# Kernel optimization log

Hardware: AMD Instinct MI355X
Metric: run time of the kernel (lower is better)

Reference implementation:

```python
import jax, jax.numpy as jnp
import numpy as np

B, C, D, H, W = 8, 16, 32, 112, 112
D_OUT, H3, W3, H2, W2 = 16, 14, 14, 7, 7
HID, OUT = 256, 128
IN_SIZE = C * H2 * W2  # 784


def setup_inputs() -> dict:
    key = jax.random.key(0)
    ks = jax.random.split(key, 8)
    s_ih = 1.0 / np.sqrt(HID)
    return {
        "x": jax.random.normal(ks[0], (B, C, D, H, W), dtype=jnp.float32),
        "W_ih": jax.random.uniform(ks[1], (3 * HID, IN_SIZE), jnp.float32, -s_ih, s_ih),
        "W_hh": jax.random.uniform(ks[2], (3 * HID, HID), jnp.float32, -s_ih, s_ih),
        "b_ih": jax.random.uniform(ks[3], (3 * HID,), jnp.float32, -s_ih, s_ih),
        "b_hh": jax.random.uniform(ks[4], (3 * HID,), jnp.float32, -s_ih, s_ih),
        "W_out": jax.random.uniform(ks[5], (OUT, HID), jnp.float32, -s_ih, s_ih),
        "b_out": jax.random.uniform(ks[6], (OUT,), jnp.float32, -s_ih, s_ih),
    }


def reference(x, W_ih, W_hh, b_ih, b_hh, W_out, b_out):
    # AdaptiveAvgPool3d (D,H,W)->(D_OUT,H3,W3): divisible factors -> mean pooling
    p3 = x.reshape(B, C, D_OUT, D // D_OUT, H3, H // H3, W3, W // W3).mean(axis=(3, 5, 7))
    # AdaptiveAvgPool2d per temporal slice (H3,W3)->(H2,W2)
    p2 = p3.reshape(B, C, D_OUT, H2, H3 // H2, W2, W3 // W2).mean(axis=(4, 6))
    # sequence over D_OUT: [T, B, C*H2*W2]
    seq = p2.transpose(2, 0, 1, 3, 4).reshape(D_OUT, B, IN_SIZE)

    def step(h, inp):
        gi = inp @ W_ih.T + b_ih  # [B, 3H]
        gh = h @ W_hh.T + b_hh    # [B, 3H]
        ir, iz, inn = jnp.split(gi, 3, axis=-1)
        hr, hz, hn = jnp.split(gh, 3, axis=-1)
        r = jax.nn.sigmoid(ir + hr)
        z = jax.nn.sigmoid(iz + hz)
        n = jnp.tanh(inn + r * hn)
        h_new = (1.0 - z) * n + z * h
        return h_new, None

    h0 = jnp.zeros((B, HID), dtype=x.dtype)
    h, _ = jax.lax.scan(step, h0, seq)
    return h @ W_out.T + b_out
```

## Files before the change

### kernel.cpp

```cpp
#include <hip/hip_runtime.h>
#include <hip/hip_bf16.h>
#include <cstdint>

#define BB 8
#define CC 16
#define DD 32
#define HH 112
#define WW 112
#define TT 16
#define HID 256
#define OUTN 128
#define INSZ 784
#define NCACHE 48

__device__ __forceinline__ float bf16lo(uint32_t u) { return __uint_as_float(u << 16); }
__device__ __forceinline__ float bf16hi(uint32_t u) { return __uint_as_float(u & 0xffff0000u); }
__device__ __forceinline__ float bf16s(uint16_t u)  { return __uint_as_float(((uint32_t)u) << 16); }

__device__ __forceinline__ uint16_t f32_to_bf16_rne(float f) {
    uint32_t u = __float_as_uint(f);
    return (uint16_t)((u + 0x7fffu + ((u >> 16) & 1u)) >> 16);
}

__global__ __launch_bounds__(256) void detect_kernel(const uint16_t* __restrict__ x,
                                                     int* __restrict__ flag) {
    __shared__ int cnt;
    if (threadIdx.x == 0) cnt = 0;
    __syncthreads();
    int local = 0;
    for (int i = threadIdx.x; i < 8192; i += 256) {
        uint32_t e = (x[i] >> 7) & 0xFFu;
        if (e == 0u || e >= 0x90u) local++;
    }
    atomicAdd(&cnt, local);
    __syncthreads();
    if (threadIdx.x == 0) *flag = (cnt > 400) ? 1 : 0;
}

__global__ __launch_bounds__(256) void pool_kernel(const void* __restrict__ xv,
                                                   float* __restrict__ seq,
                                                   const int* __restrict__ flag) {
    const int isf32 = *flag;
    int gid = blockIdx.x;
    int t = gid & 15, c = (gid >> 4) & 15, b = gid >> 8;
    long base = (long)(((b * CC + c) * DD) + t * 2) * (HH * WW);
    __shared__ float chunk[6272];
    int tid = threadIdx.x;
    float s = 0.0f;
    if (!isf32) {
        const uint4* p = reinterpret_cast<const uint4*>((const uint16_t*)xv + base);
        for (int m = tid; m < 3136; m += 256) {
            uint4 v = p[m];
            chunk[m] = bf16lo(v.x) + bf16hi(v.x) + bf16lo(v.y) + bf16hi(v.y)
                     + bf16lo(v.z) + bf16hi(v.z) + bf16lo(v.w) + bf16hi(v.w);
        }
        __syncthreads();
        if (tid < 49) {
            int h2 = tid / 7, w2 = tid - h2 * 7;
            #pragma unroll
            for (int d = 0; d < 2; d++)
                for (int hh = 0; hh < 16; hh++) {
                    int row = d * 1568 + (h2 * 16 + hh) * 14 + w2 * 2;
                    s += chunk[row] + chunk[row + 1];
                }
        }
    } else {
        const float4* p = reinterpret_cast<const float4*>((const float*)xv + base);
        for (int m = tid; m < 6272; m += 256) {
            float4 v = p[m];
            chunk[m] = v.x + v.y + v.z + v.w;
        }
        __syncthreads();
        if (tid < 49) {
            int h2 = tid / 7, w2 = tid - h2 * 7;
            #pragma unroll
            for (int d = 0; d < 2; d++)
                for (int hh = 0; hh < 16; hh++) {
                    int row = d * 3136 + (h2 * 16 + hh) * 28 + w2 * 4;
                    s += chunk[row] + chunk[row + 1] + chunk[row + 2] + chunk[row + 3];
                }
        }
    }
    if (tid < 49) {
        seq[(long)(t * BB + b) * INSZ + c * 49 + tid] = s * (1.0f / 512.0f);
    }
}

__global__ __launch_bounds__(256) void pack_all(const void* __restrict__ Wih,
                                                float* __restrict__ wihT,
                                                const void* __restrict__ Whh,
                                                uint32_t* __restrict__ whhP,
                                                const void* __restrict__ bih,
                                                float* __restrict__ gi,
                                                const int* __restrict__ flag) {
    const int isf32 = *flag;
    const int blk = blockIdx.x;
    const int tid = threadIdx.x;
    __shared__ float tlds[64][65];
    if (blk < 156) {
        int jt = blk / 13, kt = blk - jt * 13;
        int j0 = jt * 64, k0 = kt * 64;
        int rr = tid >> 6, c = tid & 63;
        #pragma unroll
        for (int r0 = 0; r0 < 64; r0 += 4) {
            int jL = r0 + rr;
            int k = k0 + c;
            if (k < INSZ) {
                long idx = (long)(j0 + jL) * INSZ + k;
                tlds[jL][c] = isf32 ? ((const float*)Wih)[idx]
                                    : bf16s(((const uint16_t*)Wih)[idx]);
            }
        }
        __syncthreads();
        #pragma unroll
        for (int r0 = 0; r0 < 64; r0 += 4) {
            int kL = r0 + rr;
            int k = k0 + kL;
            if (k < INSZ) {
                wihT[(long)k * 768 + j0 + c] = tlds[c][kL];
            }
        }
    } else if (blk < 540) {
        int g = (blk - 156) * 256 + tid;
        int jr = g >> 7, kk = g & 127;
        uint32_t u;
        if (isf32) {
            float2 v = ((const float2*)Whh)[g];
            u = (uint32_t)f32_to_bf16_rne(v.x) | ((uint32_t)f32_to_bf16_rne(v.y) << 16);
        } else {
            u = ((const uint32_t*)Whh)[g];
        }
        whhP[kk * 768 + jr] = u;
    } else {
        int g = (blk - 540) * 256 + tid;
        int jj = g % 768;
        float bv = isf32 ? ((const float*)bih)[jj] : bf16s(((const uint16_t*)bih)[jj]);
        gi[g] = bv;
    }
}

__global__ __launch_bounds__(256) void gi_kernel(const float* __restrict__ seq,
                                                 const float* __restrict__ wihT,
                                                 float* __restrict__ gi) {
    int jg = blockIdx.x % 3;
    int tbg = (blockIdx.x / 3) & 31;
    int kh = blockIdx.x / 96;
    int tb0 = tbg * 4;
    int j = jg * 256 + threadIdx.x;
    int k0 = kh * 392;
    __shared__ __align__(16) float s_in[392 * 4];
    const float* sbase = seq + (long)tb0 * INSZ + k0;
    for (int idx = threadIdx.x; idx < 392 * 4; idx += 256) {
        int i = idx / 392, k = idx - i * 392;
        s_in[k * 4 + i] = sbase[(long)i * INSZ + k];
    }
    __syncthreads();
    float a0 = 0.0f, a1 = 0.0f, a2 = 0.0f, a3 = 0.0f;
    const float* wp = wihT + (long)k0 * 768 + j;
    const float4* s4 = reinterpret_cast<const float4*>(s_in);
    #pragma unroll 8
    for (int k = 0; k < 392; k++) {
        float w = wp[(long)k * 768];
        float4 sv = s4[k];
        a0 += w * sv.x; a1 += w * sv.y; a2 += w * sv.z; a3 += w * sv.w;
    }
    atomicAdd(&gi[(long)(tb0 + 0) * 768 + j], a0);
    atomicAdd(&gi[(long)(tb0 + 1) * 768 + j], a1);
    atomicAdd(&gi[(long)(tb0 + 2) * 768 + j], a2);
    atomicAdd(&gi[(long)(tb0 + 3) * 768 + j], a3);
}

__global__ __launch_bounds__(768) void gru_kernel(const float* __restrict__ gi,
                                                  const uint32_t* __restrict__ whhP,
                                                  const void* __restrict__ bhh,
                                                  const void* __restrict__ Wout,
                                                  const void* __restrict__ bout,
                                                  void* __restrict__ out,
                                                  const int* __restrict__ flag) {
    const int isf32 = *flag;
    int b = blockIdx.x;
    int j = threadIdx.x;
    __shared__ __align__(16) float h_s[HID];
    __shared__ __align__(16) float g_s[768];
    __shared__ __align__(16) uint32_t w_s[NCACHE * 768];
    if (j < HID) h_s[j] = 0.0f;
    float bh = isf32 ? ((const float*)bhh)[j] : bf16s(((const uint16_t*)bhh)[j]);
    for (int idx = j; idx < NCACHE * 768; idx += 768) w_s[idx] = whhP[idx];
    const uint32_t* wpg = whhP + (long)NCACHE * 768 + j;
    const uint32_t* wls = w_s + j;
    __syncthreads();
    #pragma unroll 1
    for (int t = 0; t < TT; t++) {
        float a0 = bh, a1 = 0.0f;
        const float2* h2p = reinterpret_cast<const float2*>(h_s);
        #pragma unroll 8
        for (int kk = 0; kk < 128 - NCACHE; kk++) {
            uint32_t u = wpg[kk * 768];
            float2 hv = h2p[NCACHE + kk];
            a0 += bf16lo(u) * hv.x;
            a1 += bf16hi(u) * hv.y;
        }
        #pragma unroll 8
        for (int kk = 0; kk < NCACHE; kk++) {
            uint32_t u = wls[kk * 768];
            float2 hv = h2p[kk];
            a0 += bf16lo(u) * hv.x;
            a1 += bf16hi(u) * hv.y;
        }
        g_s[j] = a0 + a1;
        __syncthreads();
        if (j < HID) {
            const float* gp = gi + (long)(t * BB + b) * 768;
            float r = 1.0f / (1.0f + __expf(-(gp[j]       + g_s[j])));
            float z = 1.0f / (1.0f + __expf(-(gp[j + 256] + g_s[j + 256])));
            float npre = gp[j + 512] + r * g_s[j + 512];
            float n = 2.0f / (1.0f + __expf(-2.0f * npre)) - 1.0f;
            h_s[j] = (1.0f - z) * n + z * h_s[j];
        }
        __syncthreads();
    }
    if (j < OUTN) {
        float acc = isf32 ? ((const float*)bout)[j] : bf16s(((const uint16_t*)bout)[j]);
        if (!isf32) {
            const uint4* wo = reinterpret_cast<const uint4*>((const uint16_t*)Wout + (long)j * HID);
            #pragma unroll
            for (int k = 0; k < 32; k++) {
                uint4 v = wo[k];
                const float* hp2 = &h_s[k * 8];
                acc += bf16lo(v.x) * hp2[0] + bf16hi(v.x) * hp2[1]
                     + bf16lo(v.y) * hp2[2] + bf16hi(v.y) * hp2[3]
                     + bf16lo(v.z) * hp2[4] + bf16hi(v.z) * hp2[5]
                     + bf16lo(v.w) * hp2[6] + bf16hi(v.w) * hp2[7];
            }
            ((uint16_t*)out)[b * OUTN + j] = f32_to_bf16_rne(acc);
        } else {
            const float4* wo = reinterpret_cast<const float4*>((const float*)Wout + (long)j * HID);
            #pragma unroll
            for (int k = 0; k < 64; k++) {
                float4 v = wo[k];
                const float* hp2 = &h_s[k * 4];
                acc += v.x * hp2[0] + v.y * hp2[1] + v.z * hp2[2] + v.w * hp2[3];
            }
            ((float*)out)[b * OUTN + j] = acc;
        }
    }
}

extern "C" void kernel_launch(void* const* d_in, const int* in_sizes, int n_in,
                              void* d_out, int out_size, void* d_ws, size_t ws_size,
                              hipStream_t stream) {
    const void* x    = d_in[0];
    const void* Wih  = d_in[1];
    const void* Whh  = d_in[2];
    const void* bih  = d_in[3];
    const void* bhh  = d_in[4];
    const void* Wout = d_in[5];
    const void* bout = d_in[6];

    char* ws = (char*)d_ws;
    float*    seq  = (float*)ws;
    float*    gi   = (float*)(ws + 401408);
    float*    wihT = (float*)(ws + 1048576);
    uint32_t* whhP = (uint32_t*)(ws + 4194304);
    int*     flagp = (int*)(ws + 8388608);

    detect_kernel<<<1, 256, 0, stream>>>((const uint16_t*)x, flagp);
    pool_kernel<<<2048, 256, 0, stream>>>(x, seq, flagp);
    pack_all<<<924, 256, 0, stream>>>(Wih, wihT, Whh, whhP, bih, gi, flagp);
    gi_kernel<<<192, 256, 0, stream>>>(seq, wihT, gi);
    gru_kernel<<<8, 768, 0, stream>>>(gi, whhP, bhh, Wout, bout, d_out, flagp);
}
```

Measured before the change: 405.9 us.

## Merge pooling and weight packing into one launch; keep GRU recurrent weights in registers

Combines the pooling kernel and the weight/bias packing kernel into one grid, indexed by block range, so one launch and its inter-kernel gap disappear and packing blocks can run alongside pooling. The GRU kernel now loads the 80 non-LDS-cached W_hh columns into per-thread registers once, instead of re-reading them from global memory on each of the 16 timesteps. The added launch_bounds minimum-blocks hint and the 80-element register array raise register pressure with 768 threads per block, which could cause spills.

New measurement: 413.4 us. About the same (+1.8%).

```diff
diff --git a/kernel.cpp b/kernel.cpp
--- a/kernel.cpp
+++ b/kernel.cpp
@@ -12,6 +12,7 @@
 #define OUTN 128
 #define INSZ 784
 #define NCACHE 48
+#define NREG (128 - NCACHE)
 
 __device__ __forceinline__ float bf16lo(uint32_t u) { return __uint_as_float(u << 16); }
 __device__ __forceinline__ float bf16hi(uint32_t u) { return __uint_as_float(u & 0xffff0000u); }
@@ -37,68 +38,63 @@
     if (threadIdx.x == 0) *flag = (cnt > 400) ? 1 : 0;
 }
 
-__global__ __launch_bounds__(256) void pool_kernel(const void* __restrict__ xv,
-                                                   float* __restrict__ seq,
-                                                   const int* __restrict__ flag) {
-    const int isf32 = *flag;
-    int gid = blockIdx.x;
-    int t = gid & 15, c = (gid >> 4) & 15, b = gid >> 8;
-    long base = (long)(((b * CC + c) * DD) + t * 2) * (HH * WW);
-    __shared__ float chunk[6272];
-    int tid = threadIdx.x;
-    float s = 0.0f;
-    if (!isf32) {
-        const uint4* p = reinterpret_cast<const uint4*>((const uint16_t*)xv + base);
-        for (int m = tid; m < 3136; m += 256) {
-            uint4 v = p[m];
-            chunk[m] = bf16lo(v.x) + bf16hi(v.x) + bf16lo(v.y) + bf16hi(v.y)
-                     + bf16lo(v.z) + bf16hi(v.z) + bf16lo(v.w) + bf16hi(v.w);
-        }
-        __syncthreads();
-        if (tid < 49) {
-            int h2 = tid / 7, w2 = tid - h2 * 7;
-            #pragma unroll
-            for (int d = 0; d < 2; d++)
-                for (int hh = 0; hh < 16; hh++) {
-                    int row = d * 1568 + (h2 * 16 + hh) * 14 + w2 * 2;
-                    s += chunk[row] + chunk[row + 1];
-                }
-        }
-    } else {
-        const float4* p = reinterpret_cast<const float4*>((const float*)xv + base);
-        for (int m = tid; m < 6272; m += 256) {
-            float4 v = p[m];
-            chunk[m] = v.x + v.y + v.z + v.w;
-        }
-        __syncthreads();
-        if (tid < 49) {
-            int h2 = tid / 7, w2 = tid - h2 * 7;
-            #pragma unroll
-            for (int d = 0; d < 2; d++)
-                for (int hh = 0; hh < 16; hh++) {
-                    int row = d * 3136 + (h2 * 16 + hh) * 28 + w2 * 4;
-                    s += chunk[row] + chunk[row + 1] + chunk[row + 2] + chunk[row + 3];
-                }
-        }
-    }
-    if (tid < 49) {
-        seq[(long)(t * BB + b) * INSZ + c * 49 + tid] = s * (1.0f / 512.0f);
-    }
-}
-
-__global__ __launch_bounds__(256) void pack_all(const void* __restrict__ Wih,
-                                                float* __restrict__ wihT,
-                                                const void* __restrict__ Whh,
-                                                uint32_t* __restrict__ whhP,
-                                                const void* __restrict__ bih,
-                                                float* __restrict__ gi,
-                                                const int* __restrict__ flag) {
+__global__ __launch_bounds__(256) void prep2_kernel(const void* __restrict__ xv,
+                                                    float* __restrict__ seq,
+                                                    const void* __restrict__ Wih,
+                                                    float* __restrict__ wihT,
+                                                    const void* __restrict__ Whh,
+                                                    uint32_t* __restrict__ whhP,
+                                                    const void* __restrict__ bih,
+                                                    float* __restrict__ gi,
+                                                    const int* __restrict__ flag) {
     const int isf32 = *flag;
     const int blk = blockIdx.x;
     const int tid = threadIdx.x;
-    __shared__ float tlds[64][65];
-    if (blk < 156) {
-        int jt = blk / 13, kt = blk - jt * 13;
+    __shared__ float chunk[6272];
+    if (blk < 2048) {
+        int t = blk & 15, c = (blk >> 4) & 15, b = blk >> 8;
+        long base = (long)(((b * CC + c) * DD) + t * 2) * (HH * WW);
+        float s = 0.0f;
+        if (!isf32) {
+            const uint4* p = reinterpret_cast<const uint4*>((const uint16_t*)xv + base);
+            for (int m = tid; m < 3136; m += 256) {
+                uint4 v = p[m];
+                chunk[m] = bf16lo(v.x) + bf16hi(v.x) + bf16lo(v.y) + bf16hi(v.y)
+                         + bf16lo(v.z) + bf16hi(v.z) + bf16lo(v.w) + bf16hi(v.w);
+            }
+            __syncthreads();
+            if (tid < 49) {
+                int h2 = tid / 7, w2 = tid - h2 * 7;
+                #pragma unroll
+                for (int d = 0; d < 2; d++)
+                    for (int hh = 0; hh < 16; hh++) {
+                        int row = d * 1568 + (h2 * 16 + hh) * 14 + w2 * 2;
+                        s += chunk[row] + chunk[row + 1];
+                    }
+            }
+        } else {
+            const float4* p = reinterpret_cast<const float4*>((const float*)xv + base);
+            for (int m = tid; m < 6272; m += 256) {
+                float4 v = p[m];
+                chunk[m] = v.x + v.y + v.z + v.w;
+            }
+            __syncthreads();
+            if (tid < 49) {
+                int h2 = tid / 7, w2 = tid - h2 * 7;
+                #pragma unroll
+                for (int d = 0; d < 2; d++)
+                    for (int hh = 0; hh < 16; hh++) {
+                        int row = d * 3136 + (h2 * 16 + hh) * 28 + w2 * 4;
+                        s += chunk[row] + chunk[row + 1] + chunk[row + 2] + chunk[row + 3];
+                    }
+            }
+        }
+        if (tid < 49) {
+            seq[(long)(t * BB + b) * INSZ + c * 49 + tid] = s * (1.0f / 512.0f);
+        }
+    } else if (blk < 2204) {
+        int blk2 = blk - 2048;
+        int jt = blk2 / 13, kt = blk2 - jt * 13;
         int j0 = jt * 64, k0 = kt * 64;
         int rr = tid >> 6, c = tid & 63;
         #pragma unroll
@@ -107,8 +103,8 @@
             int k = k0 + c;
             if (k < INSZ) {
                 long idx = (long)(j0 + jL) * INSZ + k;
-                tlds[jL][c] = isf32 ? ((const float*)Wih)[idx]
-                                    : bf16s(((const uint16_t*)Wih)[idx]);
+                chunk[jL * 65 + c] = isf32 ? ((const float*)Wih)[idx]
+                                           : bf16s(((const uint16_t*)Wih)[idx]);
             }
         }
         __syncthreads();
@@ -117,11 +113,11 @@
             int kL = r0 + rr;
             int k = k0 + kL;
             if (k < INSZ) {
-                wihT[(long)k * 768 + j0 + c] = tlds[c][kL];
-            }
-        }
-    } else if (blk < 540) {
-        int g = (blk - 156) * 256 + tid;
+                wihT[(long)k * 768 + j0 + c] = chunk[c * 65 + kL];
+            }
+        }
+    } else if (blk < 2588) {
+        int g = (blk - 2204) * 256 + tid;
         int jr = g >> 7, kk = g & 127;
         uint32_t u;
         if (isf32) {
@@ -132,7 +128,7 @@
         }
         whhP[kk * 768 + jr] = u;
     } else {
-        int g = (blk - 540) * 256 + tid;
+        int g = (blk - 2588) * 256 + tid;
         int jj = g % 768;
         float bv = isf32 ? ((const float*)bih)[jj] : bf16s(((const uint16_t*)bih)[jj]);
         gi[g] = bv;
@@ -170,13 +166,13 @@
     atomicAdd(&gi[(long)(tb0 + 3) * 768 + j], a3);
 }
 
-__global__ __launch_bounds__(768) void gru_kernel(const float* __restrict__ gi,
-                                                  const uint32_t* __restrict__ whhP,
-                                                  const void* __restrict__ bhh,
-                                                  const void* __restrict__ Wout,
-                                                  const void* __restrict__ bout,
-                                                  void* __restrict__ out,
-                                                  const int* __restrict__ flag) {
+__global__ __launch_bounds__(768, 3) void gru_kernel(const float* __restrict__ gi,
+                                                     const uint32_t* __restrict__ whhP,
+                                                     const void* __restrict__ bhh,
+                                                     const void* __restrict__ Wout,
+                                                     const void* __restrict__ bout,
+                                                     void* __restrict__ out,
+                                                     const int* __restrict__ flag) {
     const int isf32 = *flag;
     int b = blockIdx.x;
     int j = threadIdx.x;
@@ -188,14 +184,17 @@
     for (int idx = j; idx < NCACHE * 768; idx += 768) w_s[idx] = whhP[idx];
     const uint32_t* wpg = whhP + (long)NCACHE * 768 + j;
     const uint32_t* wls = w_s + j;
+    uint32_t wreg[NREG];
+    #pragma unroll
+    for (int kk = 0; kk < NREG; kk++) wreg[kk] = wpg[kk * 768];
     __syncthreads();
     #pragma unroll 1
     for (int t = 0; t < TT; t++) {
         float a0 = bh, a1 = 0.0f;
         const float2* h2p = reinterpret_cast<const float2*>(h_s);
-        #pragma unroll 8
-        for (int kk = 0; kk < 128 - NCACHE; kk++) {
-            uint32_t u = wpg[kk * 768];
+        #pragma unroll
+        for (int kk = 0; kk < NREG; kk++) {
+            uint32_t u = wreg[kk];
             float2 hv = h2p[NCACHE + kk];
             a0 += bf16lo(u) * hv.x;
             a1 += bf16hi(u) * hv.y;
@@ -265,8 +264,7 @@
     int*     flagp = (int*)(ws + 8388608);
 
     detect_kernel<<<1, 256, 0, stream>>>((const uint16_t*)x, flagp);
-    pool_kernel<<<2048, 256, 0, stream>>>(x, seq, flagp);
-    pack_all<<<924, 256, 0, stream>>>(Wih, wihT, Whh, whhP, bih, gi, flagp);
+    prep2_kernel<<<2972, 256, 0, stream>>>(x, seq, Wih, wihT, Whh, whhP, bih, gi, flagp);
     gi_kernel<<<192, 256, 0, stream>>>(seq, wihT, gi);
     gru_kernel<<<8, 768, 0, stream>>>(gi, whhP, bhh, Wout, bout, d_out, flagp);
 }
```
